# Optimization experiments

Measured on AMD Instinct MI355X. Metric: run time of the kernel, lower is better.

## Reference

```python
import jax, jax.numpy as jnp
import numpy as np

B = 1024          # batch
INPUT_LEN = 4096  # dense width of incoming activation
OUT = 4096        # out_features
FAN_IN = 128      # in_features (fixed fan-in per output)


def setup_inputs() -> dict:
    key = jax.random.key(0)
    k1, k2, k3, k4 = jax.random.split(key, 4)
    bound = 1.0 / np.sqrt(FAN_IN)
    inp = jax.random.normal(k1, (B, INPUT_LEN), dtype=jnp.float32)
    weight = jax.random.uniform(k2, (OUT, FAN_IN), dtype=jnp.float32, minval=-bound, maxval=bound)
    bias = jax.random.uniform(k3, (OUT,), dtype=jnp.float32, minval=-bound, maxval=bound)
    indx_seqs = jax.random.randint(k4, (OUT, FAN_IN), 0, INPUT_LEN, dtype=jnp.int64 if jax.config.jax_enable_x64 else jnp.int32)
    return {"input": inp, "weight": weight, "bias": bias, "indx_seqs": indx_seqs}


def reference(input, weight, bias, indx_seqs):
    # gathered: (B, OUT, FAN_IN); weight broadcast over batch; reduce fan-in.
    gathered = input[:, indx_seqs]
    out = jnp.einsum('of,bof->bo', weight, gathered) + bias
    return out
```

## Files before the change

kernel.cpp:

```cpp
#include <hip/hip_runtime.h>
#include <hip/hip_fp16.h>
#include <stdint.h>

#define NB    1024
#define IL    4096
#define NOUT  4096
#define FI    128
#define BTILE 8
#define OSPLIT 4
#define OTILE (NOUT / OSPLIT)
#define SLAB_DW (IL * (BTILE / 2))
#define SLAB_BLOCKS ((NB / BTILE) * IL / 256)
#define SORT_BLOCKS (NOUT / 4)

typedef _Float16 h2v __attribute__((ext_vector_type(2)));
__device__ __forceinline__ h2v as_h2(uint32_t u){ union{uint32_t u; h2v h;} c; c.u=u; return c.h; }
#if __has_builtin(__builtin_amdgcn_fdot2)
__device__ __forceinline__ float fdot2(h2v a, h2v b, float c){ return __builtin_amdgcn_fdot2(a,b,c,false); }
#else
__device__ __forceinline__ float fdot2(h2v a, h2v b, float c){ return c + (float)a[0]*(float)b[0] + (float)a[1]*(float)b[1]; }
#endif

__device__ __forceinline__ uint32_t f16bits(float x) {
  return (uint32_t)__half_as_ushort(__float2half(x));
}

__global__ __launch_bounds__(256)
void prep_kernel(const float* __restrict__ in, uint32_t* __restrict__ slab,
                 const int* __restrict__ idx, const float* __restrict__ w,
                 uint2* __restrict__ pack2) {
  __shared__ uint32_t sbuf[4][FI];
  const int bid = blockIdx.x;
  if (bid < SLAB_BLOCKS) {
    int t = bid * 256 + threadIdx.x;
    int g = t >> 12;
    int i = t & (IL - 1);
    const float* base = in + (size_t)g * (8 * IL) + i;
    uint4 v;
    v.x = (f16bits(base[1 * IL]) << 16) | f16bits(base[0 * IL]);
    v.y = (f16bits(base[3 * IL]) << 16) | f16bits(base[2 * IL]);
    v.z = (f16bits(base[5 * IL]) << 16) | f16bits(base[4 * IL]);
    v.w = (f16bits(base[7 * IL]) << 16) | f16bits(base[6 * IL]);
    reinterpret_cast<uint4*>(slab)[t] = v;
  } else {
    const int wv = threadIdx.x >> 6;
    const int o = (bid - SLAB_BLOCKS) * 4 + wv;
    const unsigned lane = threadIdx.x & 63u;
    const uint32_t r = (uint32_t)(o & 7);
    const int*   irow = idx + (size_t)o * FI;
    const float* wrow = w   + (size_t)o * FI;

    uint32_t i0 = (uint32_t)irow[lane], i1 = (uint32_t)irow[64 + lane];
    uint32_t e0 = (f16bits(wrow[lane])      << 16) | ((i0 << 4) & 0xFFFFu);
    uint32_t e1 = (f16bits(wrow[64 + lane]) << 16) | ((i1 << 4) & 0xFFFFu);
    uint32_t k0 = i0 & 7u, k1 = i1 & 7u;
    const uint64_t lt = (1ull << lane) - 1ull;

    uint32_t rank0 = 0, rank1 = 0;
    uint64_t cntp = 0;
    #pragma unroll
    for (int g = 0; g < 8; ++g) {
      uint64_t b0 = __ballot(k0 == (uint32_t)g);
      uint64_t b1 = __ballot(k1 == (uint32_t)g);
      uint32_t c0 = (uint32_t)__popcll(b0);
      if (k0 == (uint32_t)g) rank0 = (uint32_t)__popcll(b0 & lt);
      if (k1 == (uint32_t)g) rank1 = c0 + (uint32_t)__popcll(b1 & lt);
      cntp |= (uint64_t)(c0 + (uint32_t)__popcll(b1)) << (8 * g);
    }
    uint64_t ov0 = __ballot(rank0 >= 16u);
    uint64_t ov1 = __ballot(rank1 >= 16u);
    uint32_t ofr0 = (uint32_t)__popcll(ov0 & lt);
    uint32_t ofr1 = (uint32_t)__popcll(ov0) + (uint32_t)__popcll(ov1 & lt);

    auto place = [&](uint32_t k, uint32_t rank, uint32_t ofr) -> uint32_t {
      if (rank < 16u) return ((k - r) & 7u) + 8u * rank;
      uint32_t cum = 0, p = 0;
      bool done = false;
      #pragma unroll
      for (int lc = 0; lc < 8; ++lc) {
        uint32_t gl = ((uint32_t)lc + r) & 7u;
        uint32_t c  = (uint32_t)((cntp >> (8 * gl)) & 0xFFu);
        uint32_t u  = c < 16u ? c : 16u;
        uint32_t lcnt = 16u - u;
        if (!done && ofr < cum + lcnt) { p = (uint32_t)lc + 8u * (u + ofr - cum); done = true; }
        cum += lcnt;
      }
      return p;
    };
    sbuf[wv][place(k0, rank0, ofr0)] = e0;
    sbuf[wv][place(k1, rank1, ofr1)] = e1;
    __syncthreads();

    uint32_t s0 = sbuf[wv][2 * lane], s1 = sbuf[wv][2 * lane + 1];
    uint2 pe;
    pe.x = ((s0 & 0xFFFFu) << 16) | (s1 & 0xFFFFu);
    pe.y = (s1 & 0xFFFF0000u) | (s0 >> 16);
    pack2[(size_t)o * 64 + lane] = pe;
  }
}

__device__ __forceinline__ void stage_slab(const uint32_t* src, uint32_t* lds, int tid) {
  #pragma unroll
  for (int r = 0; r < 4; ++r) {
    int e = (r * 1024 + tid) * 4;
    __builtin_amdgcn_global_load_lds(
        (const __attribute__((address_space(1))) uint32_t*)(src + e),
        (__attribute__((address_space(3))) uint32_t*)(lds + e),
        16, 0, 0);
  }
}

__global__ __launch_bounds__(1024)
void lincond_kernel(const uint32_t* __restrict__ slab,
                    const uint2* __restrict__ pack2,
                    const float* __restrict__ bias,
                    float* __restrict__ out) {
  __shared__ uint32_t lds[SLAB_DW];
  const int bid   = blockIdx.x;
  const int b0    = (bid >> 2) * BTILE;
  const int obase = (bid & 3) * OTILE;
  const int tid   = threadIdx.x;
  stage_slab(slab + (size_t)(b0 >> 3) * SLAB_DW, lds, tid);
  __syncthreads();

  const int o = obase + tid;
  const char* ldsb = reinterpret_cast<const char*>(lds);
  float acc[8] = {0.f,0.f,0.f,0.f,0.f,0.f,0.f,0.f};
  const uint4* pw4 = reinterpret_cast<const uint4*>(pack2) + (size_t)o * 32;

#define DOT2P(U1, U2, WT, K0, K1) {                                             \
    acc[K0] = fdot2(as_h2(__builtin_amdgcn_perm((U2), (U1), 0x05040100u)),      \
                    as_h2(WT), acc[K0]);                                        \
    acc[K1] = fdot2(as_h2(__builtin_amdgcn_perm((U2), (U1), 0x07060302u)),      \
                    as_h2(WT), acc[K1]);}

#define ENTRY(AD, WT) {                                                         \
    uint32_t a1 = (AD) >> 16, a2 = (AD) & 0xFFFFu;                              \
    uint4 g1 = *reinterpret_cast<const uint4*>(ldsb + a1);                      \
    uint4 g2 = *reinterpret_cast<const uint4*>(ldsb + a2);                      \
    DOT2P(g1.x, g2.x, WT, 0, 1)                                                 \
    DOT2P(g1.y, g2.y, WT, 2, 3)                                                 \
    DOT2P(g1.z, g2.z, WT, 4, 5)                                                 \
    DOT2P(g1.w, g2.w, WT, 6, 7)}

  #pragma unroll 2
  for (int j = 0; j < 8; ++j) {
    uint4 pq[4];
    #pragma unroll
    for (int q = 0; q < 4; ++q) pq[q] = pw4[j * 4 + q];
    #pragma unroll
    for (int q = 0; q < 4; ++q) {
      ENTRY(pq[q].x, pq[q].y)
      ENTRY(pq[q].z, pq[q].w)
    }
  }

  const float bv = bias[o];
  #pragma unroll
  for (int k = 0; k < 8; ++k)
    out[(size_t)(b0 + k) * NOUT + o] = acc[k] + bv;
}

__global__ __launch_bounds__(256)
void lincond_raw(const float* __restrict__ input, const float* __restrict__ wgt,
                 const float* __restrict__ bias, const int* __restrict__ idxs,
                 float* __restrict__ out) {
  int t = blockIdx.x * 256 + threadIdx.x;
  int b = t >> 12, o = t & (NOUT - 1);
  const float* irow = input + (size_t)b * IL;
  const int*   ix   = idxs + (size_t)o * FI;
  const float* wr   = wgt  + (size_t)o * FI;
  float acc = bias[o];
  for (int f = 0; f < FI; ++f) acc += wr[f] * irow[ix[f]];
  out[t] = acc;
}

extern "C" void kernel_launch(void* const* d_in, const int* in_sizes, int n_in,
                              void* d_out, int out_size, void* d_ws, size_t ws_size,
                              hipStream_t stream) {
  const float* input  = (const float*)d_in[0];
  const float* weight = (const float*)d_in[1];
  const float* bias   = (const float*)d_in[2];
  const int*   idxs   = (const int*)d_in[3];
  float*       out    = (float*)d_out;

  const size_t pack_bytes = (size_t)NOUT * 64 * sizeof(uint2);
  const size_t slab_bytes = (size_t)(NB / BTILE) * SLAB_DW * sizeof(uint32_t);
  const int grid = (NB / BTILE) * OSPLIT;

  if (ws_size >= pack_bytes + slab_bytes) {
    uint2*    pack2 = (uint2*)d_ws;
    uint32_t* slab  = (uint32_t*)((char*)d_ws + pack_bytes);
    prep_kernel<<<SLAB_BLOCKS + SORT_BLOCKS, 256, 0, stream>>>(input, slab, idxs, weight, pack2);
    lincond_kernel<<<grid, 1024, 0, stream>>>(slab, pack2, bias, out);
  } else {
    lincond_raw<<<(NB * NOUT) / 256, 256, 0, stream>>>(input, weight, bias, idxs, out);
  }
}
```

Baseline: 52.94 us.

## Halve block size, give each thread two outputs with software-pipelined LDS reads

Measured after the change: 52.02 us. No clear change (-1.7%).

```diff
diff --git a/kernel.cpp b/kernel.cpp
--- a/kernel.cpp
+++ b/kernel.cpp
@@ -99,18 +99,7 @@
   }
 }
 
-__device__ __forceinline__ void stage_slab(const uint32_t* src, uint32_t* lds, int tid) {
-  #pragma unroll
-  for (int r = 0; r < 4; ++r) {
-    int e = (r * 1024 + tid) * 4;
-    __builtin_amdgcn_global_load_lds(
-        (const __attribute__((address_space(1))) uint32_t*)(src + e),
-        (__attribute__((address_space(3))) uint32_t*)(lds + e),
-        16, 0, 0);
-  }
-}
-
-__global__ __launch_bounds__(1024)
+__global__ __launch_bounds__(512, 4)
 void lincond_kernel(const uint32_t* __restrict__ slab,
                     const uint2* __restrict__ pack2,
                     const float* __restrict__ bias,
@@ -120,45 +109,81 @@
   const int b0    = (bid >> 2) * BTILE;
   const int obase = (bid & 3) * OTILE;
   const int tid   = threadIdx.x;
-  stage_slab(slab + (size_t)(b0 >> 3) * SLAB_DW, lds, tid);
+
+  {
+    const uint32_t* src = slab + (size_t)(b0 >> 3) * SLAB_DW;
+    #pragma unroll
+    for (int r = 0; r < 8; ++r) {
+      int e = (r * 512 + tid) * 4;
+      __builtin_amdgcn_global_load_lds(
+          (const __attribute__((address_space(1))) uint32_t*)(src + e),
+          (__attribute__((address_space(3))) uint32_t*)(lds + e),
+          16, 0, 0);
+    }
+  }
   __syncthreads();
 
-  const int o = obase + tid;
+  const int oA = obase + tid;
+  const int oB = oA + 512;
   const char* ldsb = reinterpret_cast<const char*>(lds);
-  float acc[8] = {0.f,0.f,0.f,0.f,0.f,0.f,0.f,0.f};
-  const uint4* pw4 = reinterpret_cast<const uint4*>(pack2) + (size_t)o * 32;
-
-#define DOT2P(U1, U2, WT, K0, K1) {                                             \
-    acc[K0] = fdot2(as_h2(__builtin_amdgcn_perm((U2), (U1), 0x05040100u)),      \
-                    as_h2(WT), acc[K0]);                                        \
-    acc[K1] = fdot2(as_h2(__builtin_amdgcn_perm((U2), (U1), 0x07060302u)),      \
-                    as_h2(WT), acc[K1]);}
-
-#define ENTRY(AD, WT) {                                                         \
-    uint32_t a1 = (AD) >> 16, a2 = (AD) & 0xFFFFu;                              \
-    uint4 g1 = *reinterpret_cast<const uint4*>(ldsb + a1);                      \
-    uint4 g2 = *reinterpret_cast<const uint4*>(ldsb + a2);                      \
-    DOT2P(g1.x, g2.x, WT, 0, 1)                                                 \
-    DOT2P(g1.y, g2.y, WT, 2, 3)                                                 \
-    DOT2P(g1.z, g2.z, WT, 4, 5)                                                 \
-    DOT2P(g1.w, g2.w, WT, 6, 7)}
-
-  #pragma unroll 2
+  float accA[8] = {0.f,0.f,0.f,0.f,0.f,0.f,0.f,0.f};
+  float accB[8] = {0.f,0.f,0.f,0.f,0.f,0.f,0.f,0.f};
+  const uint4* pwA = reinterpret_cast<const uint4*>(pack2) + (size_t)oA * 32;
+  const uint4* pwB = reinterpret_cast<const uint4*>(pack2) + (size_t)oB * 32;
+
+#define RD2(AD, G1, G2) {                                                       \
+    uint32_t a1_ = (AD) >> 16, a2_ = (AD) & 0xFFFFu;                            \
+    G1 = *reinterpret_cast<const uint4*>(ldsb + a1_);                           \
+    G2 = *reinterpret_cast<const uint4*>(ldsb + a2_); }
+
+#define DOT2P(ACC, U1, U2, WT, K0, K1) {                                        \
+    ACC[K0] = fdot2(as_h2(__builtin_amdgcn_perm((U2), (U1), 0x05040100u)),      \
+                    as_h2(WT), ACC[K0]);                                        \
+    ACC[K1] = fdot2(as_h2(__builtin_amdgcn_perm((U2), (U1), 0x07060302u)),      \
+                    as_h2(WT), ACC[K1]);}
+
+#define CONS(ACC, G1, G2, WT) {                                                 \
+    DOT2P(ACC, (G1).x, (G2).x, WT, 0, 1)                                        \
+    DOT2P(ACC, (G1).y, (G2).y, WT, 2, 3)                                        \
+    DOT2P(ACC, (G1).z, (G2).z, WT, 4, 5)                                        \
+    DOT2P(ACC, (G1).w, (G2).w, WT, 6, 7)}
+
+  #pragma unroll 1
   for (int j = 0; j < 8; ++j) {
-    uint4 pq[4];
-    #pragma unroll
-    for (int q = 0; q < 4; ++q) pq[q] = pw4[j * 4 + q];
-    #pragma unroll
-    for (int q = 0; q < 4; ++q) {
-      ENTRY(pq[q].x, pq[q].y)
-      ENTRY(pq[q].z, pq[q].w)
-    }
-  }
-
-  const float bv = bias[o];
+    uint4 pA0 = pwA[j * 4 + 0], pA1 = pwA[j * 4 + 1];
+    uint4 pA2 = pwA[j * 4 + 2], pA3 = pwA[j * 4 + 3];
+    uint4 pB0 = pwB[j * 4 + 0], pB1 = pwB[j * 4 + 1];
+    uint4 pB2 = pwB[j * 4 + 2], pB3 = pwB[j * 4 + 3];
+
+    uint4 aA1, aA2, bA1, bA2;
+    uint4 aB1, aB2, bB1, bB2;
+
+    RD2(pA0.x, aA1, aA2);  RD2(pB0.x, aB1, aB2);
+    RD2(pA0.z, bA1, bA2);  CONS(accA, aA1, aA2, pA0.y);
+    RD2(pB0.z, bB1, bB2);  CONS(accB, aB1, aB2, pB0.y);
+    RD2(pA1.x, aA1, aA2);  CONS(accA, bA1, bA2, pA0.w);
+    RD2(pB1.x, aB1, aB2);  CONS(accB, bB1, bB2, pB0.w);
+    RD2(pA1.z, bA1, bA2);  CONS(accA, aA1, aA2, pA1.y);
+    RD2(pB1.z, bB1, bB2);  CONS(accB, aB1, aB2, pB1.y);
+    RD2(pA2.x, aA1, aA2);  CONS(accA, bA1, bA2, pA1.w);
+    RD2(pB2.x, aB1, aB2);  CONS(accB, bB1, bB2, pB1.w);
+    RD2(pA2.z, bA1, bA2);  CONS(accA, aA1, aA2, pA2.y);
+    RD2(pB2.z, bB1, bB2);  CONS(accB, aB1, aB2, pB2.y);
+    RD2(pA3.x, aA1, aA2);  CONS(accA, bA1, bA2, pA2.w);
+    RD2(pB3.x, aB1, aB2);  CONS(accB, bB1, bB2, pB2.w);
+    RD2(pA3.z, bA1, bA2);  CONS(accA, aA1, aA2, pA3.y);
+    RD2(pB3.z, bB1, bB2);  CONS(accB, aB1, aB2, pB3.y);
+                           CONS(accA, bA1, bA2, pA3.w);
+                           CONS(accB, bB1, bB2, pB3.w);
+  }
+
+  const float bvA = bias[oA];
+  const float bvB = bias[oB];
   #pragma unroll
-  for (int k = 0; k < 8; ++k)
-    out[(size_t)(b0 + k) * NOUT + o] = acc[k] + bv;
+  for (int k = 0; k < 8; ++k) {
+    out[(size_t)(b0 + k) * NOUT + oA] = accA[k] + bvA;
+    out[(size_t)(b0 + k) * NOUT + oB] = accB[k] + bvB;
+  }
 }
 
 __global__ __launch_bounds__(256)
@@ -192,7 +217,7 @@
     uint2*    pack2 = (uint2*)d_ws;
     uint32_t* slab  = (uint32_t*)((char*)d_ws + pack_bytes);
     prep_kernel<<<SLAB_BLOCKS + SORT_BLOCKS, 256, 0, stream>>>(input, slab, idxs, weight, pack2);
-    lincond_kernel<<<grid, 1024, 0, stream>>>(slab, pack2, bias, out);
+    lincond_kernel<<<grid, 512, 0, stream>>>(slab, pack2, bias, out);
   } else {
     lincond_raw<<<(NB * NOUT) / 256, 256, 0, stream>>>(input, weight, bias, idxs, out);
   }
```

## Software-pipeline LDS gathers with inline ds_read and halve block size

Applied to the files above, without the earlier changes.

Result: slower. 57.68 us (+8.9%).

```diff
diff --git a/kernel.cpp b/kernel.cpp
--- a/kernel.cpp
+++ b/kernel.cpp
@@ -7,13 +7,14 @@
 #define NOUT  4096
 #define FI    128
 #define BTILE 8
-#define OSPLIT 4
+#define OSPLIT 8
 #define OTILE (NOUT / OSPLIT)
 #define SLAB_DW (IL * (BTILE / 2))
 #define SLAB_BLOCKS ((NB / BTILE) * IL / 256)
 #define SORT_BLOCKS (NOUT / 4)
 
 typedef _Float16 h2v __attribute__((ext_vector_type(2)));
+typedef uint32_t u32x4 __attribute__((ext_vector_type(4)));
 __device__ __forceinline__ h2v as_h2(uint32_t u){ union{uint32_t u; h2v h;} c; c.u=u; return c.h; }
 #if __has_builtin(__builtin_amdgcn_fdot2)
 __device__ __forceinline__ float fdot2(h2v a, h2v b, float c){ return __builtin_amdgcn_fdot2(a,b,c,false); }
@@ -99,34 +100,42 @@
   }
 }
 
-__device__ __forceinline__ void stage_slab(const uint32_t* src, uint32_t* lds, int tid) {
-  #pragma unroll
-  for (int r = 0; r < 4; ++r) {
-    int e = (r * 1024 + tid) * 4;
-    __builtin_amdgcn_global_load_lds(
-        (const __attribute__((address_space(1))) uint32_t*)(src + e),
-        (__attribute__((address_space(3))) uint32_t*)(lds + e),
-        16, 0, 0);
-  }
-}
-
-__global__ __launch_bounds__(1024)
+__global__ __launch_bounds__(512, 4)
 void lincond_kernel(const uint32_t* __restrict__ slab,
                     const uint2* __restrict__ pack2,
                     const float* __restrict__ bias,
                     float* __restrict__ out) {
   __shared__ uint32_t lds[SLAB_DW];
   const int bid   = blockIdx.x;
-  const int b0    = (bid >> 2) * BTILE;
-  const int obase = (bid & 3) * OTILE;
+  const int b0    = (bid >> 3) * BTILE;
+  const int obase = (bid & 7) * OTILE;
   const int tid   = threadIdx.x;
-  stage_slab(slab + (size_t)(b0 >> 3) * SLAB_DW, lds, tid);
+
+  {
+    const uint32_t* src = slab + (size_t)(b0 >> 3) * SLAB_DW;
+    #pragma unroll
+    for (int r = 0; r < 8; ++r) {
+      int e = (r * 512 + tid) * 4;
+      __builtin_amdgcn_global_load_lds(
+          (const __attribute__((address_space(1))) uint32_t*)(src + e),
+          (__attribute__((address_space(3))) uint32_t*)(lds + e),
+          16, 0, 0);
+    }
+  }
   __syncthreads();
 
   const int o = obase + tid;
-  const char* ldsb = reinterpret_cast<const char*>(lds);
+  const uint32_t lb = (uint32_t)(uintptr_t)(__attribute__((address_space(3))) uint32_t*)lds;
   float acc[8] = {0.f,0.f,0.f,0.f,0.f,0.f,0.f,0.f};
   const uint4* pw4 = reinterpret_cast<const uint4*>(pack2) + (size_t)o * 32;
+
+#define DSRD2(GA, GB, AW)                                                       \
+  asm volatile("ds_read_b128 %0, %2\n\tds_read_b128 %1, %3"                     \
+    : "=v"(GA), "=v"(GB)                                                        \
+    : "v"(lb + ((AW) >> 16)), "v"(lb + ((AW) & 0xFFFFu)));
+
+#define WAITL6 { asm volatile("s_waitcnt lgkmcnt(6)" ::: "memory");             \
+                 __builtin_amdgcn_sched_barrier(0); }
 
 #define DOT2P(U1, U2, WT, K0, K1) {                                             \
     acc[K0] = fdot2(as_h2(__builtin_amdgcn_perm((U2), (U1), 0x05040100u)),      \
@@ -134,26 +143,37 @@
     acc[K1] = fdot2(as_h2(__builtin_amdgcn_perm((U2), (U1), 0x07060302u)),      \
                     as_h2(WT), acc[K1]);}
 
-#define ENTRY(AD, WT) {                                                         \
-    uint32_t a1 = (AD) >> 16, a2 = (AD) & 0xFFFFu;                              \
-    uint4 g1 = *reinterpret_cast<const uint4*>(ldsb + a1);                      \
-    uint4 g2 = *reinterpret_cast<const uint4*>(ldsb + a2);                      \
-    DOT2P(g1.x, g2.x, WT, 0, 1)                                                 \
-    DOT2P(g1.y, g2.y, WT, 2, 3)                                                 \
-    DOT2P(g1.z, g2.z, WT, 4, 5)                                                 \
-    DOT2P(g1.w, g2.w, WT, 6, 7)}
-
-  #pragma unroll 2
+#define CONS(GA, GB, WT) {                                                      \
+    DOT2P((GA)[0], (GB)[0], WT, 0, 1)                                           \
+    DOT2P((GA)[1], (GB)[1], WT, 2, 3)                                           \
+    DOT2P((GA)[2], (GB)[2], WT, 4, 5)                                           \
+    DOT2P((GA)[3], (GB)[3], WT, 6, 7)}
+
+  u32x4 s0a, s0b, s1a, s1b, s2a, s2b, s3a, s3b;
+  uint4 c0 = pw4[0], c1 = pw4[1], c2 = pw4[2], c3 = pw4[3];
+
+  DSRD2(s0a, s0b, c0.x);
+  DSRD2(s1a, s1b, c0.z);
+  DSRD2(s2a, s2b, c1.x);
+  DSRD2(s3a, s3b, c1.z);
+
+  #pragma unroll 1
   for (int j = 0; j < 8; ++j) {
-    uint4 pq[4];
-    #pragma unroll
-    for (int q = 0; q < 4; ++q) pq[q] = pw4[j * 4 + q];
-    #pragma unroll
-    for (int q = 0; q < 4; ++q) {
-      ENTRY(pq[q].x, pq[q].y)
-      ENTRY(pq[q].z, pq[q].w)
-    }
-  }
+    const int jn = ((j + 1) & 7) * 4;
+    uint4 n0 = pw4[jn + 0], n1 = pw4[jn + 1], n2 = pw4[jn + 2], n3 = pw4[jn + 3];
+
+    WAITL6 CONS(s0a, s0b, c0.y); DSRD2(s0a, s0b, c2.x);
+    WAITL6 CONS(s1a, s1b, c0.w); DSRD2(s1a, s1b, c2.z);
+    WAITL6 CONS(s2a, s2b, c1.y); DSRD2(s2a, s2b, c3.x);
+    WAITL6 CONS(s3a, s3b, c1.w); DSRD2(s3a, s3b, c3.z);
+    WAITL6 CONS(s0a, s0b, c2.y); DSRD2(s0a, s0b, n0.x);
+    WAITL6 CONS(s1a, s1b, c2.w); DSRD2(s1a, s1b, n0.z);
+    WAITL6 CONS(s2a, s2b, c3.y); DSRD2(s2a, s2b, n1.x);
+    WAITL6 CONS(s3a, s3b, c3.w); DSRD2(s3a, s3b, n1.z);
+
+    c0 = n0; c1 = n1; c2 = n2; c3 = n3;
+  }
+  asm volatile("s_waitcnt lgkmcnt(0)" ::: "memory");
 
   const float bv = bias[o];
   #pragma unroll
@@ -192,7 +212,7 @@
     uint2*    pack2 = (uint2*)d_ws;
     uint32_t* slab  = (uint32_t*)((char*)d_ws + pack_bytes);
     prep_kernel<<<SLAB_BLOCKS + SORT_BLOCKS, 256, 0, stream>>>(input, slab, idxs, weight, pack2);
-    lincond_kernel<<<grid, 1024, 0, stream>>>(slab, pack2, bias, out);
+    lincond_kernel<<<grid, 512, 0, stream>>>(slab, pack2, bias, out);
   } else {
     lincond_raw<<<(NB * NOUT) / 256, 256, 0, stream>>>(input, weight, bias, idxs, out);
   }
```
